# Performance work log

Measured on AMD Instinct MI355X. Metric: run time of the kernel, lower is better.

## Reference

```python
import jax, jax.numpy as jnp
import numpy as np

N, F, H, C, E, L = 100000, 512, 64, 40, 1600000, 6


def setup_inputs() -> dict:
    key = jax.random.key(0)
    ks = jax.random.split(key, 2 * L + 4)
    x = jax.random.normal(ks[0], (N, F), dtype=jnp.float32)
    edge_index = jax.random.randint(ks[1], (2, E), 0, N, dtype=jnp.int32)
    inp = {"x": x, "edge_index": edge_index}
    in_dims = [F + H * i for i in range(L)]  # 512, 576, ..., 832 (dense concat)
    for i in range(L):
        inp[f"W{i}"] = jax.random.normal(ks[2 + i], (in_dims[i], H), dtype=jnp.float32) / np.sqrt(in_dims[i]).astype(np.float32)
        inp[f"b{i}"] = jnp.zeros((H,), dtype=jnp.float32)
    jk_dim = in_dims[-1] + H  # 896 = num_features + 6*H
    inp["Wlin"] = jax.random.normal(ks[2 + L], (jk_dim, C), dtype=jnp.float32) / np.sqrt(jk_dim).astype(np.float32)
    inp["blin"] = jnp.zeros((C,), dtype=jnp.float32)
    return inp


def _gcn_norm(edge_index, num_nodes, dtype):
    # Add self loops, compute symmetric normalization deg^-1/2 * deg^-1/2
    loop = jnp.arange(num_nodes, dtype=edge_index.dtype)
    row = jnp.concatenate([edge_index[0], loop])  # source
    col = jnp.concatenate([edge_index[1], loop])  # target
    deg = jax.ops.segment_sum(jnp.ones_like(col, dtype=dtype), col, num_segments=num_nodes)
    dinv = jnp.where(deg > 0, jax.lax.rsqrt(jnp.maximum(deg, 1.0)), 0.0)
    norm = dinv[row] * dinv[col]  # [E + N]
    return row, col, norm


def reference(x, edge_index, W0, b0, W1, b1, W2, b2, W3, b3, W4, b4, W5, b5, Wlin, blin):
    Ws = [W0, W1, W2, W3, W4, W5]
    bs = [b0, b1, b2, b3, b4, b5]
    n = x.shape[0]
    row, col, norm = _gcn_norm(edge_index, n, x.dtype)

    xs = [x]
    for W, b in zip(Ws, bs):
        inp = jnp.concatenate(xs, axis=1)          # dense (DenseNet-style) concat
        lin = inp @ W                               # [n, H] transform before propagate
        msg = lin[row] * norm[:, None]              # gather + edge weight
        agg = jax.ops.segment_sum(msg, col, num_segments=n)  # scatter-add aggregate
        h = jax.nn.relu(agg + b)                    # GCNConv bias, then ReLU (dropout = eval mode)
        xs.append(h)

    hcat = jnp.concatenate(xs, axis=1)              # JumpingKnowledge('cat')
    logits = hcat @ Wlin + blin
    return jax.nn.log_softmax(logits, axis=1)
```

## Files before the change

### kernel.cpp

```cpp
#include <hip/hip_runtime.h>
#include <hip/hip_bf16.h>

#define HH 64
#define XDIM 896
#define FF 512
#define LL 6
#define CC 40
#define CBSZ 512
#define SLACK 10240

typedef __bf16 bf16x8 __attribute__((ext_vector_type(8)));
typedef float f32x4 __attribute__((ext_vector_type(4)));

__device__ __forceinline__ unsigned short f2bf(float f){
  union{float f; unsigned int u;} v; v.f=f; unsigned int u=v.u;
  return (unsigned short)((u + 0x7fffu + ((u>>16)&1u))>>16);
}
__device__ __forceinline__ float u2f(unsigned u){
  union{unsigned u; float f;} v; v.u=u; return v.f;
}

struct PrepP {
  const float* x; const int* ei;
  unsigned short* X; unsigned short* lin;
  int* bcur; unsigned* tmp;
  const float* W[7]; unsigned short* dst[7];
  int nt[7], nc[7], off[8];
  int N, E, CH, NB, WB;
};

__global__ void __launch_bounds__(256) k_prep(PrepP P){
  __shared__ int hist[256];
  __shared__ int run[256];
  int t=threadIdx.x, b=blockIdx.x;
  if (b < 256){
    int E=P.E;
    int lo=b*P.CH, hi=lo+P.CH; if (hi>E) hi=E;
    for (int i=t;i<P.NB;i+=256) hist[i]=0;
    __syncthreads();
    for (int i=lo+t;i<hi;i+=256) atomicAdd(&hist[P.ei[E+i]>>9], 1);
    __syncthreads();
    for (int i=t;i<P.NB;i+=256) run[i]=i*SLACK+atomicAdd(&P.bcur[i], hist[i]);
    __syncthreads();
    for (int i=lo+t;i<hi;i+=256){
      int r=P.ei[i], c=P.ei[E+i];
      int pos=atomicAdd(&run[c>>9],1);
      P.tmp[pos]=((unsigned)r<<9)|(unsigned)(c&(CBSZ-1));
    }
  } else if (b < 256+P.WB){
    int idx=(b-256)*256+t;
    if (idx < P.off[7]){
      int seg=0;
      while (idx>=P.off[seg+1]) ++seg;
      int li=idx-P.off[seg];
      int j=li&7, ln=(li>>3)&63, rem2=li>>9;
      int ntile=P.nt[seg], ncols=P.nc[seg];
      int nt=rem2%ntile, kb=rem2/ntile;
      int k=kb*32+(ln>>4)*8+j;
      int c=nt*16+(ln&15);
      float v=(c<ncols)? P.W[seg][(size_t)k*ncols+c] : 0.f;
      P.dst[seg][li]=f2bf(v);
    }
  } else {
    int i=(b-256-P.WB)*256+t;
    if (i<32) ((unsigned*)(P.lin+(size_t)P.N*64))[i]=0u;
    int total=P.N*(FF/4);
    if (i<total){
      int row=i/(FF/4), c4=(i%(FF/4))*4;
      float4 v=*(const float4*)(P.x+(size_t)row*FF+c4);
      ushort4 o; o.x=f2bf(v.x); o.y=f2bf(v.y); o.z=f2bf(v.z); o.w=f2bf(v.w);
      *(ushort4*)(P.X+(size_t)row*XDIM+c4)=o;
    }
  }
}

__global__ void __launch_bounds__(1024) k_build(const unsigned* __restrict__ tmp,
                                                const int* __restrict__ bcur,
                                                int* __restrict__ offsS, int* __restrict__ offsE,
                                                float* __restrict__ dinv,
                                                int* __restrict__ esrc, int N){
  __shared__ int cnt[CBSZ];
  __shared__ int run[CBSZ];
  int t=threadIdx.x, b=blockIdx.x;
  int n0=b*CBSZ;
  int nloc=N-n0; if (nloc>CBSZ) nloc=CBSZ;
  int wbase=b*SLACK;
  int wend=wbase + bcur[b];
  if (t<CBSZ) cnt[t]=0;
  __syncthreads();
  for (int i=wbase+t; i<wend; i+=1024) atomicAdd(&cnt[tmp[i]&(CBSZ-1u)],1);
  __syncthreads();
  int v = (t<CBSZ)? cnt[t] : 0;
  if (t<CBSZ) run[t]=v;
  __syncthreads();
  for (int o=1;o<CBSZ;o<<=1){
    int xx = (t<CBSZ && t>=o)? run[t-o] : 0;
    __syncthreads();
    if (t<CBSZ) run[t]+=xx;
    __syncthreads();
  }
  if (t<nloc){
    int s = wbase + (run[t]-v);
    offsS[n0+t]=s;
    offsE[n0+t]=s+v;
    dinv[n0+t]=rsqrtf((float)(v+1));
    run[t]=s;
  }
  __syncthreads();
  for (int i=wbase+t; i<wend; i+=1024){
    unsigned vv=tmp[i];
    int pos=atomicAdd(&run[vv&(CBSZ-1u)],1);
    esrc[pos]=(int)(vv>>9);
  }
}

__global__ void __launch_bounds__(256) k_gemm(const unsigned short* __restrict__ X,
                                              const unsigned short* __restrict__ Wf,
                                              const float* __restrict__ dinv,
                                              unsigned short* __restrict__ lin,
                                              int N, int nkb){
  int lane = threadIdx.x & 63, wid = threadIdx.x >> 6;
  long row0 = (long)blockIdx.x*128 + wid*32;
  int arow = lane & 15, kgrp = lane >> 4;
  long r0 = row0 + arow;      if (r0 > (long)N-1) r0 = N-1;
  long r1 = row0 + 16 + arow; if (r1 > (long)N-1) r1 = N-1;
  const unsigned short* ap0 = X + (size_t)r0*XDIM + kgrp*8;
  const unsigned short* ap1 = X + (size_t)r1*XDIM + kgrp*8;
  const unsigned short* bptr = Wf + lane*8;
  f32x4 acc00={0.f,0.f,0.f,0.f}, acc01=acc00, acc02=acc00, acc03=acc00;
  f32x4 acc10=acc00, acc11=acc00, acc12=acc00, acc13=acc00;
  for (int kb=0; kb<nkb; ++kb){
    bf16x8 a0 = *(const bf16x8*)(ap0 + (size_t)kb*32);
    bf16x8 a1 = *(const bf16x8*)(ap1 + (size_t)kb*32);
    const unsigned short* bp = bptr + (size_t)kb*2048;
    bf16x8 b0=*(const bf16x8*)bp, b1=*(const bf16x8*)(bp+512),
           b2=*(const bf16x8*)(bp+1024), b3=*(const bf16x8*)(bp+1536);
    acc00=__builtin_amdgcn_mfma_f32_16x16x32_bf16(a0,b0,acc00,0,0,0);
    acc10=__builtin_amdgcn_mfma_f32_16x16x32_bf16(a1,b0,acc10,0,0,0);
    acc01=__builtin_amdgcn_mfma_f32_16x16x32_bf16(a0,b1,acc01,0,0,0);
    acc11=__builtin_amdgcn_mfma_f32_16x16x32_bf16(a1,b1,acc11,0,0,0);
    acc02=__builtin_amdgcn_mfma_f32_16x16x32_bf16(a0,b2,acc02,0,0,0);
    acc12=__builtin_amdgcn_mfma_f32_16x16x32_bf16(a1,b2,acc12,0,0,0);
    acc03=__builtin_amdgcn_mfma_f32_16x16x32_bf16(a0,b3,acc03,0,0,0);
    acc13=__builtin_amdgcn_mfma_f32_16x16x32_bf16(a1,b3,acc13,0,0,0);
  }
  for (int j=0;j<4;++j){
    long rr = row0 + kgrp*4 + j;
    if (rr < N){
      float dv = dinv[rr];
      unsigned short* lp = lin + (size_t)rr*64 + arow;
      lp[0]  = f2bf(acc00[j]*dv);
      lp[16] = f2bf(acc01[j]*dv);
      lp[32] = f2bf(acc02[j]*dv);
      lp[48] = f2bf(acc03[j]*dv);
    }
    long rr1 = rr + 16;
    if (rr1 < N){
      float dv = dinv[rr1];
      unsigned short* lp = lin + (size_t)rr1*64 + arow;
      lp[0]  = f2bf(acc10[j]*dv);
      lp[16] = f2bf(acc11[j]*dv);
      lp[32] = f2bf(acc12[j]*dv);
      lp[48] = f2bf(acc13[j]*dv);
    }
  }
}

#define AGG_UNPACK(v) \
  a0 += u2f(v.x<<16); a1 += u2f(v.x&0xffff0000u); \
  a2 += u2f(v.y<<16); a3 += u2f(v.y&0xffff0000u); \
  a4 += u2f(v.z<<16); a5 += u2f(v.z&0xffff0000u); \
  a6 += u2f(v.w<<16); a7 += u2f(v.w&0xffff0000u);

#define AGG_TIER(NG) \
  _Pragma("unroll") \
  for (int k=0;k<NG;++k){ \
    int idx = 8*k + sub; \
    int sx = esrc[base + idx]; \
    sx = (idx < rem) ? sx : N; \
    uint4 v = *(const uint4*)(lq + (size_t)sx*64); \
    AGG_UNPACK(v) \
  }

__global__ void __launch_bounds__(256) k_agg(const unsigned short* __restrict__ lin,
                                             const int* __restrict__ offsS,
                                             const int* __restrict__ offsE,
                                             const int* __restrict__ esrc,
                                             const float* __restrict__ dinv,
                                             const float* __restrict__ bias,
                                             unsigned short* __restrict__ X,
                                             int colbase, int N){
  int lane = threadIdx.x & 63, wid = threadIdx.x >> 6;
  int n = blockIdx.x*4 + wid;
  if (n >= N) return;
  int sub = lane >> 3;
  int fq  = lane & 7;
  const unsigned short* lq = lin + fq*8;
  float a0=0.f,a1=0.f,a2=0.f,a3=0.f,a4=0.f,a5=0.f,a6=0.f,a7=0.f;
  int s = offsS[n], e = offsE[n];
  int base = s;
  for (; base + 64 <= e; base += 64){
    #pragma unroll
    for (int k=0;k<8;++k){
      int sx = esrc[base + 8*k + sub];
      uint4 v = *(const uint4*)(lq + (size_t)sx*64);
      AGG_UNPACK(v)
    }
  }
  if (base < e){
    int rem = e - base;
    if      (rem <=  8) { AGG_TIER(1) }
    else if (rem <= 16) { AGG_TIER(2) }
    else if (rem <= 24) { AGG_TIER(3) }
    else if (rem <= 32) { AGG_TIER(4) }
    else if (rem <= 48) { AGG_TIER(6) }
    else                { AGG_TIER(8) }
  }
  a0 += __shfl_xor(a0,8,64); a0 += __shfl_xor(a0,16,64); a0 += __shfl_xor(a0,32,64);
  a1 += __shfl_xor(a1,8,64); a1 += __shfl_xor(a1,16,64); a1 += __shfl_xor(a1,32,64);
  a2 += __shfl_xor(a2,8,64); a2 += __shfl_xor(a2,16,64); a2 += __shfl_xor(a2,32,64);
  a3 += __shfl_xor(a3,8,64); a3 += __shfl_xor(a3,16,64); a3 += __shfl_xor(a3,32,64);
  a4 += __shfl_xor(a4,8,64); a4 += __shfl_xor(a4,16,64); a4 += __shfl_xor(a4,32,64);
  a5 += __shfl_xor(a5,8,64); a5 += __shfl_xor(a5,16,64); a5 += __shfl_xor(a5,32,64);
  a6 += __shfl_xor(a6,8,64); a6 += __shfl_xor(a6,16,64); a6 += __shfl_xor(a6,32,64);
  a7 += __shfl_xor(a7,8,64); a7 += __shfl_xor(a7,16,64); a7 += __shfl_xor(a7,32,64);
  uint4 vs = *(const uint4*)(lq + (size_t)n*64);
  AGG_UNPACK(vs)
  float dv = dinv[n];
  float4 bA = *(const float4*)(bias + fq*8);
  float4 bB = *(const float4*)(bias + fq*8 + 4);
  float h0 = fmaxf(a0*dv + bA.x, 0.f);
  float h1 = fmaxf(a1*dv + bA.y, 0.f);
  float h2 = fmaxf(a2*dv + bA.z, 0.f);
  float h3 = fmaxf(a3*dv + bA.w, 0.f);
  float h4 = fmaxf(a4*dv + bB.x, 0.f);
  float h5 = fmaxf(a5*dv + bB.y, 0.f);
  float h6 = fmaxf(a6*dv + bB.z, 0.f);
  float h7 = fmaxf(a7*dv + bB.w, 0.f);
  if (sub == 0){
    uint4 o;
    o.x = (unsigned)f2bf(h0) | ((unsigned)f2bf(h1)<<16);
    o.y = (unsigned)f2bf(h2) | ((unsigned)f2bf(h3)<<16);
    o.z = (unsigned)f2bf(h4) | ((unsigned)f2bf(h5)<<16);
    o.w = (unsigned)f2bf(h6) | ((unsigned)f2bf(h7)<<16);
    *(uint4*)(X + (size_t)n*XDIM + colbase + fq*8) = o;
  }
}

__global__ void __launch_bounds__(256) k_final(const unsigned short* __restrict__ X,
                                               const unsigned short* __restrict__ Wf,
                                               const float* __restrict__ blin,
                                               float* __restrict__ out, int N){
  int lane=threadIdx.x&63, wid=threadIdx.x>>6;
  long row0=(long)blockIdx.x*64 + wid*16;
  int c0=lane&15, g=lane>>4;
  long r=row0+c0; if (r > (long)N-1) r = N-1;
  const unsigned short* aptr = X + (size_t)r*XDIM + g*8;
  const unsigned short* bptr = Wf + lane*8;
  f32x4 acc0={0.f,0.f,0.f,0.f}, acc1=acc0, acc2=acc0;
  const int nkb = XDIM/32;
  for (int kb=0;kb<nkb;++kb){
    bf16x8 a=*(const bf16x8*)(aptr+(size_t)kb*32);
    const unsigned short* bp = bptr + (size_t)kb*1536;
    bf16x8 b0=*(const bf16x8*)bp, b1=*(const bf16x8*)(bp+512), b2=*(const bf16x8*)(bp+1024);
    acc0=__builtin_amdgcn_mfma_f32_16x16x32_bf16(a,b0,acc0,0,0,0);
    acc1=__builtin_amdgcn_mfma_f32_16x16x32_bf16(a,b1,acc1,0,0,0);
    acc2=__builtin_amdgcn_mfma_f32_16x16x32_bf16(a,b2,acc2,0,0,0);
  }
  float bl0 = blin[c0], bl1 = blin[16+c0];
  bool v2ok = (c0 < 8);
  float bl2 = v2ok ? blin[32+c0] : 0.f;
  for (int j=0;j<4;++j){
    long rr = row0 + g*4 + j;
    float v0 = acc0[j]+bl0, v1 = acc1[j]+bl1;
    float v2 = v2ok ? (acc2[j]+bl2) : -1e30f;
    float m = fmaxf(fmaxf(v0,v1),v2);
    m = fmaxf(m, __shfl_xor(m,1,64));
    m = fmaxf(m, __shfl_xor(m,2,64));
    m = fmaxf(m, __shfl_xor(m,4,64));
    m = fmaxf(m, __shfl_xor(m,8,64));
    float sEx = expf(v0-m)+expf(v1-m)+(v2ok?expf(v2-m):0.f);
    sEx += __shfl_xor(sEx,1,64);
    sEx += __shfl_xor(sEx,2,64);
    sEx += __shfl_xor(sEx,4,64);
    sEx += __shfl_xor(sEx,8,64);
    float lse = m + logf(sEx);
    if (rr < N){
      out[(size_t)rr*CC + c0]      = v0 - lse;
      out[(size_t)rr*CC + 16 + c0] = v1 - lse;
      if (v2ok) out[(size_t)rr*CC + 32 + c0] = v2 - lse;
    }
  }
}

extern "C" void kernel_launch(void* const* d_in, const int* in_sizes, int n_in,
                              void* d_out, int out_size, void* d_ws, size_t ws_size,
                              hipStream_t stream){
  const float* x = (const float*)d_in[0];
  const int* ei = (const int*)d_in[1];
  const float* Wl[LL]; const float* bl[LL];
  for (int i=0;i<LL;i++){ Wl[i]=(const float*)d_in[2+2*i]; bl[i]=(const float*)d_in[3+2*i]; }
  const float* Wlin = (const float*)d_in[2+2*LL];
  const float* blin = (const float*)d_in[3+2*LL];
  float* out = (float*)d_out;
  const int N = in_sizes[0]/FF;
  const int E = in_sizes[1]/2;
  const int NB = (N+CBSZ-1)/CBSZ;

  char* p = (char*)d_ws;
  auto alloc = [&](size_t bb)->char*{ char* r=p; p += (bb+255)&~(size_t)255; return r; };
  unsigned short* X   = (unsigned short*)alloc((size_t)N*XDIM*2);
  unsigned short* lin = (unsigned short*)alloc((size_t)(N+1)*64*2);
  unsigned* tmp = (unsigned*)lin;
  unsigned short* WfL[LL+1];
  for (int i=0;i<LL;i++){ int d=FF+HH*i; WfL[i]=(unsigned short*)alloc((size_t)d*64*2); }
  WfL[LL] = (unsigned short*)alloc((size_t)XDIM*48*2);
  float* dinv  = (float*)alloc((size_t)N*4);
  int* offsS   = (int*)alloc((size_t)N*4);
  int* offsE   = (int*)alloc((size_t)N*4);
  int* bcur    = (int*)alloc((size_t)NB*4);
  int* esrc    = (int*)alloc(((size_t)NB*SLACK+64)*4);

  PrepP P;
  P.x=x; P.ei=ei; P.X=X; P.lin=lin; P.bcur=bcur; P.tmp=tmp;
  int off=0;
  for (int i=0;i<LL;i++){
    P.W[i]=Wl[i]; P.dst[i]=WfL[i]; P.nt[i]=4; P.nc[i]=HH;
    P.off[i]=off; off += ((FF+HH*i)>>5)*4*512;
  }
  P.W[LL]=Wlin; P.dst[LL]=WfL[LL]; P.nt[LL]=3; P.nc[LL]=CC;
  P.off[LL]=off; off += (XDIM>>5)*3*512;
  P.off[LL+1]=off;
  P.N=N; P.E=E; P.CH=(E+255)/256; P.NB=NB; P.WB=(off+255)/256;
  int XB=(N*(FF/4)+255)/256;

  hipMemsetAsync(bcur, 0, (size_t)NB*4, stream);
  k_prep <<<256 + P.WB + XB, 256, 0, stream>>>(P);
  k_build<<<NB, 1024, 0, stream>>>(tmp, bcur, offsS, offsE, dinv, esrc, N);

  int gb = (N+127)/128;
  int ab = (N+3)/4;
  for (int i=0;i<LL;i++){
    k_gemm<<<gb,256,0,stream>>>(X, WfL[i], dinv, lin, N, (FF+HH*i)>>5);
    k_agg <<<ab,256,0,stream>>>(lin, offsS, offsE, esrc, dinv, bl[i], X, FF+HH*i, N);
  }
  k_final<<<(N+63)/64,256,0,stream>>>(X, WfL[LL], blin, out, N);
}
```

Before: 657.3 us.

## Fuse per-layer aggregation with next layer's GEMM via shared-memory tile

Each layer's aggregation is merged with the following layer's transform GEMM in one kernel. A block aggregates 128 nodes into shared memory, and the GEMM then reads the newest 64 columns from LDS instead of global memory. Ping-pong lin buffers are added so the next layer can write while neighbours are still being read, and the final layer's aggregation is fused with the classifier and log-softmax. This removes separate launches and the re-read of the freshly written columns. The cost is that aggregation now uses one wave per node with a 4-element lane split and 32 nodes serially per wave, which may lower memory-level parallelism.

```diff
diff --git a/kernel.cpp b/kernel.cpp
--- a/kernel.cpp
+++ b/kernel.cpp
@@ -8,6 +8,8 @@
 #define CC 40
 #define CBSZ 512
 #define SLACK 10240
+#define NPB 128
+#define HPAD 72
 
 typedef __bf16 bf16x8 __attribute__((ext_vector_type(8)));
 typedef float f32x4 __attribute__((ext_vector_type(4)));
@@ -22,7 +24,7 @@
 
 struct PrepP {
   const float* x; const int* ei;
-  unsigned short* X; unsigned short* lin;
+  unsigned short* X; unsigned short* linA; unsigned short* linB;
   int* bcur; unsigned* tmp;
   const float* W[7]; unsigned short* dst[7];
   int nt[7], nc[7], off[8];
@@ -63,7 +65,10 @@
     }
   } else {
     int i=(b-256-P.WB)*256+t;
-    if (i<32) ((unsigned*)(P.lin+(size_t)P.N*64))[i]=0u;
+    if (i<32){
+      ((unsigned*)(P.linA+(size_t)P.N*64))[i]=0u;
+      ((unsigned*)(P.linB+(size_t)P.N*64))[i]=0u;
+    }
     int total=P.N*(FF/4);
     if (i<total){
       int row=i/(FF/4), c4=(i%(FF/4))*4;
@@ -166,129 +171,223 @@
   }
 }
 
-#define AGG_UNPACK(v) \
-  a0 += u2f(v.x<<16); a1 += u2f(v.x&0xffff0000u); \
-  a2 += u2f(v.y<<16); a3 += u2f(v.y&0xffff0000u); \
-  a4 += u2f(v.z<<16); a5 += u2f(v.z&0xffff0000u); \
-  a6 += u2f(v.w<<16); a7 += u2f(v.w&0xffff0000u);
-
-#define AGG_TIER(NG) \
-  _Pragma("unroll") \
-  for (int k=0;k<NG;++k){ \
-    int idx = 8*k + sub; \
-    int sx = esrc[base + idx]; \
-    sx = (idx < rem) ? sx : N; \
-    uint4 v = *(const uint4*)(lq + (size_t)sx*64); \
-    AGG_UNPACK(v) \
-  }
-
-__global__ void __launch_bounds__(256) k_agg(const unsigned short* __restrict__ lin,
-                                             const int* __restrict__ offsS,
-                                             const int* __restrict__ offsE,
-                                             const int* __restrict__ esrc,
-                                             const float* __restrict__ dinv,
-                                             const float* __restrict__ bias,
-                                             unsigned short* __restrict__ X,
-                                             int colbase, int N){
-  int lane = threadIdx.x & 63, wid = threadIdx.x >> 6;
-  int n = blockIdx.x*4 + wid;
-  if (n >= N) return;
-  int sub = lane >> 3;
-  int fq  = lane & 7;
-  const unsigned short* lq = lin + fq*8;
-  float a0=0.f,a1=0.f,a2=0.f,a3=0.f,a4=0.f,a5=0.f,a6=0.f,a7=0.f;
-  int s = offsS[n], e = offsE[n];
-  int base = s;
-  for (; base + 64 <= e; base += 64){
-    #pragma unroll
-    for (int k=0;k<8;++k){
-      int sx = esrc[base + 8*k + sub];
-      uint4 v = *(const uint4*)(lq + (size_t)sx*64);
-      AGG_UNPACK(v)
-    }
-  }
-  if (base < e){
-    int rem = e - base;
-    if      (rem <=  8) { AGG_TIER(1) }
-    else if (rem <= 16) { AGG_TIER(2) }
-    else if (rem <= 24) { AGG_TIER(3) }
-    else if (rem <= 32) { AGG_TIER(4) }
-    else if (rem <= 48) { AGG_TIER(6) }
-    else                { AGG_TIER(8) }
-  }
-  a0 += __shfl_xor(a0,8,64); a0 += __shfl_xor(a0,16,64); a0 += __shfl_xor(a0,32,64);
-  a1 += __shfl_xor(a1,8,64); a1 += __shfl_xor(a1,16,64); a1 += __shfl_xor(a1,32,64);
-  a2 += __shfl_xor(a2,8,64); a2 += __shfl_xor(a2,16,64); a2 += __shfl_xor(a2,32,64);
-  a3 += __shfl_xor(a3,8,64); a3 += __shfl_xor(a3,16,64); a3 += __shfl_xor(a3,32,64);
-  a4 += __shfl_xor(a4,8,64); a4 += __shfl_xor(a4,16,64); a4 += __shfl_xor(a4,32,64);
-  a5 += __shfl_xor(a5,8,64); a5 += __shfl_xor(a5,16,64); a5 += __shfl_xor(a5,32,64);
-  a6 += __shfl_xor(a6,8,64); a6 += __shfl_xor(a6,16,64); a6 += __shfl_xor(a6,32,64);
-  a7 += __shfl_xor(a7,8,64); a7 += __shfl_xor(a7,16,64); a7 += __shfl_xor(a7,32,64);
-  uint4 vs = *(const uint4*)(lq + (size_t)n*64);
-  AGG_UNPACK(vs)
-  float dv = dinv[n];
-  float4 bA = *(const float4*)(bias + fq*8);
-  float4 bB = *(const float4*)(bias + fq*8 + 4);
-  float h0 = fmaxf(a0*dv + bA.x, 0.f);
-  float h1 = fmaxf(a1*dv + bA.y, 0.f);
-  float h2 = fmaxf(a2*dv + bA.z, 0.f);
-  float h3 = fmaxf(a3*dv + bA.w, 0.f);
-  float h4 = fmaxf(a4*dv + bB.x, 0.f);
-  float h5 = fmaxf(a5*dv + bB.y, 0.f);
-  float h6 = fmaxf(a6*dv + bB.z, 0.f);
-  float h7 = fmaxf(a7*dv + bB.w, 0.f);
-  if (sub == 0){
-    uint4 o;
-    o.x = (unsigned)f2bf(h0) | ((unsigned)f2bf(h1)<<16);
-    o.y = (unsigned)f2bf(h2) | ((unsigned)f2bf(h3)<<16);
-    o.z = (unsigned)f2bf(h4) | ((unsigned)f2bf(h5)<<16);
-    o.w = (unsigned)f2bf(h6) | ((unsigned)f2bf(h7)<<16);
-    *(uint4*)(X + (size_t)n*XDIM + colbase + fq*8) = o;
-  }
-}
-
-__global__ void __launch_bounds__(256) k_final(const unsigned short* __restrict__ X,
+#define AGG_BODY(lqp, n_, a0,a1,a2,a3) \
+  { \
+    int s = offsS[n_], e = offsE[n_]; \
+    int base = s; \
+    for (; base + 32 <= e; base += 32){ \
+      _Pragma("unroll") \
+      for (int k=0;k<8;++k){ \
+        int sx = esrc[base + 4*k + sub]; \
+        uint2 v = *(const uint2*)(lqp + (size_t)sx*64); \
+        a0 += u2f(v.x<<16); a1 += u2f(v.x&0xffff0000u); \
+        a2 += u2f(v.y<<16); a3 += u2f(v.y&0xffff0000u); \
+      } \
+    } \
+    if (base < e){ \
+      int rem = e - base; \
+      if (rem > 16){ \
+        _Pragma("unroll") \
+        for (int k=0;k<8;++k){ \
+          int idx = 4*k + sub; \
+          int sx = esrc[base + idx]; \
+          sx = (idx < rem) ? sx : (int)N; \
+          uint2 v = *(const uint2*)(lqp + (size_t)sx*64); \
+          a0 += u2f(v.x<<16); a1 += u2f(v.x&0xffff0000u); \
+          a2 += u2f(v.y<<16); a3 += u2f(v.y&0xffff0000u); \
+        } \
+      } else { \
+        _Pragma("unroll") \
+        for (int k=0;k<4;++k){ \
+          int idx = 4*k + sub; \
+          int sx = esrc[base + idx]; \
+          sx = (idx < rem) ? sx : (int)N; \
+          uint2 v = *(const uint2*)(lqp + (size_t)sx*64); \
+          a0 += u2f(v.x<<16); a1 += u2f(v.x&0xffff0000u); \
+          a2 += u2f(v.y<<16); a3 += u2f(v.y&0xffff0000u); \
+        } \
+      } \
+    } \
+    a0 += __shfl_xor(a0,16,64); a0 += __shfl_xor(a0,32,64); \
+    a1 += __shfl_xor(a1,16,64); a1 += __shfl_xor(a1,32,64); \
+    a2 += __shfl_xor(a2,16,64); a2 += __shfl_xor(a2,32,64); \
+    a3 += __shfl_xor(a3,16,64); a3 += __shfl_xor(a3,32,64); \
+    uint2 vs = *(const uint2*)(lqp + (size_t)n_*64); \
+    a0 += u2f(vs.x<<16); a1 += u2f(vs.x&0xffff0000u); \
+    a2 += u2f(vs.y<<16); a3 += u2f(vs.y&0xffff0000u); \
+  }
+
+__global__ void __launch_bounds__(256) k_fused(const unsigned short* __restrict__ linR,
+                                               unsigned short* __restrict__ linW,
+                                               const int* __restrict__ offsS,
+                                               const int* __restrict__ offsE,
+                                               const int* __restrict__ esrc,
+                                               const float* __restrict__ dinv,
+                                               const float* __restrict__ bias,
+                                               unsigned short* __restrict__ X,
                                                const unsigned short* __restrict__ Wf,
-                                               const float* __restrict__ blin,
-                                               float* __restrict__ out, int N){
-  int lane=threadIdx.x&63, wid=threadIdx.x>>6;
-  long row0=(long)blockIdx.x*64 + wid*16;
-  int c0=lane&15, g=lane>>4;
-  long r=row0+c0; if (r > (long)N-1) r = N-1;
-  const unsigned short* aptr = X + (size_t)r*XDIM + g*8;
-  const unsigned short* bptr = Wf + lane*8;
-  f32x4 acc0={0.f,0.f,0.f,0.f}, acc1=acc0, acc2=acc0;
-  const int nkb = XDIM/32;
-  for (int kb=0;kb<nkb;++kb){
-    bf16x8 a=*(const bf16x8*)(aptr+(size_t)kb*32);
-    const unsigned short* bp = bptr + (size_t)kb*1536;
-    bf16x8 b0=*(const bf16x8*)bp, b1=*(const bf16x8*)(bp+512), b2=*(const bf16x8*)(bp+1024);
-    acc0=__builtin_amdgcn_mfma_f32_16x16x32_bf16(a,b0,acc0,0,0,0);
-    acc1=__builtin_amdgcn_mfma_f32_16x16x32_bf16(a,b1,acc1,0,0,0);
-    acc2=__builtin_amdgcn_mfma_f32_16x16x32_bf16(a,b2,acc2,0,0,0);
-  }
-  float bl0 = blin[c0], bl1 = blin[16+c0];
-  bool v2ok = (c0 < 8);
-  float bl2 = v2ok ? blin[32+c0] : 0.f;
-  for (int j=0;j<4;++j){
-    long rr = row0 + g*4 + j;
-    float v0 = acc0[j]+bl0, v1 = acc1[j]+bl1;
-    float v2 = v2ok ? (acc2[j]+bl2) : -1e30f;
-    float m = fmaxf(fmaxf(v0,v1),v2);
-    m = fmaxf(m, __shfl_xor(m,1,64));
-    m = fmaxf(m, __shfl_xor(m,2,64));
-    m = fmaxf(m, __shfl_xor(m,4,64));
-    m = fmaxf(m, __shfl_xor(m,8,64));
-    float sEx = expf(v0-m)+expf(v1-m)+(v2ok?expf(v2-m):0.f);
-    sEx += __shfl_xor(sEx,1,64);
-    sEx += __shfl_xor(sEx,2,64);
-    sEx += __shfl_xor(sEx,4,64);
-    sEx += __shfl_xor(sEx,8,64);
-    float lse = m + logf(sEx);
-    if (rr < N){
-      out[(size_t)rr*CC + c0]      = v0 - lse;
-      out[(size_t)rr*CC + 16 + c0] = v1 - lse;
-      if (v2ok) out[(size_t)rr*CC + 32 + c0] = v2 - lse;
+                                               int colbase, int nkb, int N){
+  __shared__ unsigned short sh[NPB*HPAD];
+  int t=threadIdx.x, lane=t&63, wid=t>>6;
+  int nbase = blockIdx.x*NPB;
+  int sub = lane>>4, fq = lane&15;
+  {
+    const unsigned short* lq = linR + fq*4;
+    for (int it=0; it<32; ++it){
+      int n = nbase + wid*32 + it;
+      if (n >= N) break;
+      float a0=0.f, a1=0.f, a2=0.f, a3=0.f;
+      AGG_BODY(lq, n, a0,a1,a2,a3)
+      float dv = dinv[n];
+      float4 b4 = *(const float4*)(bias + fq*4);
+      float h0 = fmaxf(a0*dv + b4.x, 0.f);
+      float h1 = fmaxf(a1*dv + b4.y, 0.f);
+      float h2 = fmaxf(a2*dv + b4.z, 0.f);
+      float h3 = fmaxf(a3*dv + b4.w, 0.f);
+      if (sub == 0){
+        ushort4 o; o.x=f2bf(h0); o.y=f2bf(h1); o.z=f2bf(h2); o.w=f2bf(h3);
+        *(ushort4*)(&sh[(n-nbase)*HPAD + fq*4]) = o;
+        *(ushort4*)(X + (size_t)n*XDIM + colbase + fq*4) = o;
+      }
+    }
+  }
+  __syncthreads();
+  {
+    int arow = lane & 15, kgrp = lane >> 4;
+    int kbh = nkb - 2;
+    long row0 = (long)nbase + wid*32;
+    long r0 = row0 + arow;      if (r0 > (long)N-1) r0 = N-1;
+    long r1 = row0 + 16 + arow; if (r1 > (long)N-1) r1 = N-1;
+    const unsigned short* ap0 = X + (size_t)r0*XDIM + kgrp*8;
+    const unsigned short* ap1 = X + (size_t)r1*XDIM + kgrp*8;
+    int l0 = (int)(r0 - nbase)*HPAD + kgrp*8;
+    int l1 = (int)(r1 - nbase)*HPAD + kgrp*8;
+    const unsigned short* bptr = Wf + lane*8;
+    f32x4 acc00={0.f,0.f,0.f,0.f}, acc01=acc00, acc02=acc00, acc03=acc00;
+    f32x4 acc10=acc00, acc11=acc00, acc12=acc00, acc13=acc00;
+    for (int kb=0; kb<nkb; ++kb){
+      bf16x8 a0, a1;
+      if (kb < kbh){
+        a0 = *(const bf16x8*)(ap0 + (size_t)kb*32);
+        a1 = *(const bf16x8*)(ap1 + (size_t)kb*32);
+      } else {
+        int c = (kb - kbh)*32;
+        a0 = *(const bf16x8*)(&sh[l0 + c]);
+        a1 = *(const bf16x8*)(&sh[l1 + c]);
+      }
+      const unsigned short* bp = bptr + (size_t)kb*2048;
+      bf16x8 b0=*(const bf16x8*)bp, b1=*(const bf16x8*)(bp+512),
+             b2=*(const bf16x8*)(bp+1024), b3=*(const bf16x8*)(bp+1536);
+      acc00=__builtin_amdgcn_mfma_f32_16x16x32_bf16(a0,b0,acc00,0,0,0);
+      acc10=__builtin_amdgcn_mfma_f32_16x16x32_bf16(a1,b0,acc10,0,0,0);
+      acc01=__builtin_amdgcn_mfma_f32_16x16x32_bf16(a0,b1,acc01,0,0,0);
+      acc11=__builtin_amdgcn_mfma_f32_16x16x32_bf16(a1,b1,acc11,0,0,0);
+      acc02=__builtin_amdgcn_mfma_f32_16x16x32_bf16(a0,b2,acc02,0,0,0);
+      acc12=__builtin_amdgcn_mfma_f32_16x16x32_bf16(a1,b2,acc12,0,0,0);
+      acc03=__builtin_amdgcn_mfma_f32_16x16x32_bf16(a0,b3,acc03,0,0,0);
+      acc13=__builtin_amdgcn_mfma_f32_16x16x32_bf16(a1,b3,acc13,0,0,0);
+    }
+    for (int j=0;j<4;++j){
+      long rr = row0 + kgrp*4 + j;
+      if (rr < N){
+        float dv = dinv[rr];
+        unsigned short* lp = linW + (size_t)rr*64 + arow;
+        lp[0]  = f2bf(acc00[j]*dv);
+        lp[16] = f2bf(acc01[j]*dv);
+        lp[32] = f2bf(acc02[j]*dv);
+        lp[48] = f2bf(acc03[j]*dv);
+      }
+      long rr1 = rr + 16;
+      if (rr1 < N){
+        float dv = dinv[rr1];
+        unsigned short* lp = linW + (size_t)rr1*64 + arow;
+        lp[0]  = f2bf(acc10[j]*dv);
+        lp[16] = f2bf(acc11[j]*dv);
+        lp[32] = f2bf(acc12[j]*dv);
+        lp[48] = f2bf(acc13[j]*dv);
+      }
+    }
+  }
+}
+
+__global__ void __launch_bounds__(256) k_ffinal(const unsigned short* __restrict__ linR,
+                                                const int* __restrict__ offsS,
+                                                const int* __restrict__ offsE,
+                                                const int* __restrict__ esrc,
+                                                const float* __restrict__ dinv,
+                                                const float* __restrict__ bias,
+                                                const unsigned short* __restrict__ X,
+                                                const unsigned short* __restrict__ Wf,
+                                                const float* __restrict__ blin,
+                                                float* __restrict__ out, int N){
+  __shared__ unsigned short sh[NPB*HPAD];
+  int t=threadIdx.x, lane=t&63, wid=t>>6;
+  int nbase = blockIdx.x*NPB;
+  int sub = lane>>4, fq = lane&15;
+  {
+    const unsigned short* lq = linR + fq*4;
+    for (int it=0; it<32; ++it){
+      int n = nbase + wid*32 + it;
+      if (n >= N) break;
+      float a0=0.f, a1=0.f, a2=0.f, a3=0.f;
+      AGG_BODY(lq, n, a0,a1,a2,a3)
+      float dv = dinv[n];
+      float4 b4 = *(const float4*)(bias + fq*4);
+      float h0 = fmaxf(a0*dv + b4.x, 0.f);
+      float h1 = fmaxf(a1*dv + b4.y, 0.f);
+      float h2 = fmaxf(a2*dv + b4.z, 0.f);
+      float h3 = fmaxf(a3*dv + b4.w, 0.f);
+      if (sub == 0){
+        ushort4 o; o.x=f2bf(h0); o.y=f2bf(h1); o.z=f2bf(h2); o.w=f2bf(h3);
+        *(ushort4*)(&sh[(n-nbase)*HPAD + fq*4]) = o;
+      }
+    }
+  }
+  __syncthreads();
+  {
+    int c0=lane&15, g=lane>>4;
+    const int nkb = XDIM/32, kbh = nkb-2;
+    for (int tt=0; tt<2; ++tt){
+      long row0 = (long)nbase + tt*64 + wid*16;
+      long r = row0+c0; if (r > (long)N-1) r = N-1;
+      const unsigned short* aptr = X + (size_t)r*XDIM + g*8;
+      int lr = (int)(r - nbase)*HPAD + g*8;
+      const unsigned short* bptr = Wf + lane*8;
+      f32x4 acc0={0.f,0.f,0.f,0.f}, acc1=acc0, acc2=acc0;
+      for (int kb=0;kb<nkb;++kb){
+        bf16x8 a;
+        if (kb < kbh) a = *(const bf16x8*)(aptr+(size_t)kb*32);
+        else          a = *(const bf16x8*)(&sh[lr + (kb-kbh)*32]);
+        const unsigned short* bp = bptr + (size_t)kb*1536;
+        bf16x8 b0=*(const bf16x8*)bp, b1=*(const bf16x8*)(bp+512), b2=*(const bf16x8*)(bp+1024);
+        acc0=__builtin_amdgcn_mfma_f32_16x16x32_bf16(a,b0,acc0,0,0,0);
+        acc1=__builtin_amdgcn_mfma_f32_16x16x32_bf16(a,b1,acc1,0,0,0);
+        acc2=__builtin_amdgcn_mfma_f32_16x16x32_bf16(a,b2,acc2,0,0,0);
+      }
+      float bl0 = blin[c0], bl1 = blin[16+c0];
+      bool v2ok = (c0 < 8);
+      float bl2 = v2ok ? blin[32+c0] : 0.f;
+      for (int j=0;j<4;++j){
+        long rr = row0 + g*4 + j;
+        float v0 = acc0[j]+bl0, v1 = acc1[j]+bl1;
+        float v2 = v2ok ? (acc2[j]+bl2) : -1e30f;
+        float m = fmaxf(fmaxf(v0,v1),v2);
+        m = fmaxf(m, __shfl_xor(m,1,64));
+        m = fmaxf(m, __shfl_xor(m,2,64));
+        m = fmaxf(m, __shfl_xor(m,4,64));
+        m = fmaxf(m, __shfl_xor(m,8,64));
+        float sEx = expf(v0-m)+expf(v1-m)+(v2ok?expf(v2-m):0.f);
+        sEx += __shfl_xor(sEx,1,64);
+        sEx += __shfl_xor(sEx,2,64);
+        sEx += __shfl_xor(sEx,4,64);
+        sEx += __shfl_xor(sEx,8,64);
+        float lse = m + logf(sEx);
+        if (rr < N){
+          out[(size_t)rr*CC + c0]      = v0 - lse;
+          out[(size_t)rr*CC + 16 + c0] = v1 - lse;
+          if (v2ok) out[(size_t)rr*CC + 32 + c0] = v2 - lse;
+        }
+      }
     }
   }
 }
@@ -309,9 +408,10 @@
 
   char* p = (char*)d_ws;
   auto alloc = [&](size_t bb)->char*{ char* r=p; p += (bb+255)&~(size_t)255; return r; };
-  unsigned short* X   = (unsigned short*)alloc((size_t)N*XDIM*2);
-  unsigned short* lin = (unsigned short*)alloc((size_t)(N+1)*64*2);
-  unsigned* tmp = (unsigned*)lin;
+  unsigned short* X    = (unsigned short*)alloc((size_t)N*XDIM*2);
+  unsigned short* linA = (unsigned short*)alloc((size_t)(N+1)*64*2);
+  unsigned short* linB = (unsigned short*)alloc((size_t)(N+1)*64*2);
+  unsigned* tmp = (unsigned*)linA;
   unsigned short* WfL[LL+1];
   for (int i=0;i<LL;i++){ int d=FF+HH*i; WfL[i]=(unsigned short*)alloc((size_t)d*64*2); }
   WfL[LL] = (unsigned short*)alloc((size_t)XDIM*48*2);
@@ -322,7 +422,7 @@
   int* esrc    = (int*)alloc(((size_t)NB*SLACK+64)*4);
 
   PrepP P;
-  P.x=x; P.ei=ei; P.X=X; P.lin=lin; P.bcur=bcur; P.tmp=tmp;
+  P.x=x; P.ei=ei; P.X=X; P.linA=linA; P.linB=linB; P.bcur=bcur; P.tmp=tmp;
   int off=0;
   for (int i=0;i<LL;i++){
     P.W[i]=Wl[i]; P.dst[i]=WfL[i]; P.nt[i]=4; P.nc[i]=HH;
@@ -338,11 +438,15 @@
   k_prep <<<256 + P.WB + XB, 256, 0, stream>>>(P);
   k_build<<<NB, 1024, 0, stream>>>(tmp, bcur, offsS, offsE, dinv, esrc, N);
 
-  int gb = (N+127)/128;
-  int ab = (N+3)/4;
-  for (int i=0;i<LL;i++){
-    k_gemm<<<gb,256,0,stream>>>(X, WfL[i], dinv, lin, N, (FF+HH*i)>>5);
-    k_agg <<<ab,256,0,stream>>>(lin, offsS, offsE, esrc, dinv, bl[i], X, FF+HH*i, N);
-  }
-  k_final<<<(N+63)/64,256,0,stream>>>(X, WfL[LL], blin, out, N);
-}
+  int fb = (N+NPB-1)/NPB;
+  k_gemm<<<fb,256,0,stream>>>(X, WfL[0], dinv, linA, N, FF>>5);
+  unsigned short* cur = linA;
+  unsigned short* oth = linB;
+  for (int i=0;i<LL-1;i++){
+    k_fused<<<fb,256,0,stream>>>(cur, oth, offsS, offsE, esrc, dinv, bl[i],
+                                 X, WfL[i+1], FF+HH*i, (FF+HH*(i+1))>>5, N);
+    unsigned short* t2 = cur; cur = oth; oth = t2;
+  }
+  k_ffinal<<<fb,256,0,stream>>>(cur, offsS, offsE, esrc, dinv, bl[LL-1],
+                                X, WfL[LL], blin, out, N);
+}
```

Result: slower. 975.6 us (+48.4%).
